# Performance work log

Hardware: AMD Instinct MI355X
Metric: run time of the kernel (lower is better)

The kernel has to match this reference:

```python
import jax, jax.numpy as jnp
import numpy as np

G = 32          # num graphs
NPG = 512       # nodes per graph
EPG = 4096      # edges per graph
DN = 128        # node/edge feat dim
DP = 64         # node identifier dim d_p
DE_ID = 64      # type identifier dim d_e
H = 768         # hidden_dim
IN_DIM = DN + 2 * DP + DE_ID  # 320


def setup_inputs() -> dict:
    key = jax.random.key(0)
    ks = jax.random.split(key, 9)
    N = G * NPG
    E = G * EPG
    x = jax.random.normal(ks[0], (N, DN), jnp.float32)
    edge_attr = jax.random.normal(ks[1], (E, DN), jnp.float32)
    P = jax.random.normal(ks[2], (N, DP), jnp.float32)  # ORF node identifiers
    E_V = jax.random.normal(ks[3], (1, DE_ID), jnp.float32) * 0.1
    E_E = jax.random.normal(ks[4], (1, DE_ID), jnp.float32) * 0.1
    W = jax.random.normal(ks[5], (H, IN_DIM), jnp.float32) / np.sqrt(IN_DIM)
    b = jnp.zeros((H,), jnp.float32)
    graph_token = jax.random.normal(ks[6], (1, H), jnp.float32) * 0.1
    # edges stay within their graph and are sorted by graph id
    base = jnp.repeat(jnp.arange(G, dtype=jnp.int32) * NPG, EPG)  # [E]
    src = base + jax.random.randint(ks[7], (E,), 0, NPG, jnp.int32)
    dst = base + jax.random.randint(ks[8], (E,), 0, NPG, jnp.int32)
    edge_index = jnp.stack([src, dst], axis=0)  # [2, E]
    batch = jnp.repeat(jnp.arange(G, dtype=jnp.int32), NPG)  # [N]
    return {
        "x": x, "edge_attr": edge_attr, "P": P,
        "E_V": E_V, "E_E": E_E, "W": W, "b": b, "graph_token": graph_token,
        "edge_index": edge_index, "batch": batch,
        "num_graphs": G, "max_node_num": NPG, "max_edge_num": EPG,
    }


def reference(x, edge_attr, P, E_V, E_E, W, b, graph_token,
              edge_index, batch, num_graphs, max_node_num, max_edge_num):
    N = x.shape[0]
    E = edge_index.shape[1]
    Hd = W.shape[0]
    d_e = E_V.shape[1]

    # node tokens: [x | P | P | E_V] @ W^T + b
    X_v = jnp.concatenate([x, P, P, jnp.broadcast_to(E_V, (N, d_e))], axis=1)
    X_v_proj = X_v @ W.T + b  # [N, H]

    # edge tokens: [edge_attr | P_u | P_v | E_E] @ W^T + b
    P_u = P[edge_index[0]]
    P_v = P[edge_index[1]]
    X_e = jnp.concatenate([edge_attr, P_u, P_v, jnp.broadcast_to(E_E, (E, d_e))], axis=1)
    X_e_proj = X_e @ W.T + b  # [E, H]

    # ragged -> padded packing (replaces per-graph python loop)
    ones_n = jnp.ones((N,), jnp.int32)
    node_num = jax.ops.segment_sum(ones_n, batch, num_segments=num_graphs)  # [G]
    node_ptr = jnp.cumsum(node_num) - node_num  # exclusive prefix sum
    node_pos = jnp.arange(N, dtype=jnp.int32) - node_ptr[batch]  # position within graph

    edge_batch = batch[edge_index[0]]  # [E]
    ones_e = jnp.ones((E,), jnp.int32)
    edge_num = jax.ops.segment_sum(ones_e, edge_batch, num_segments=num_graphs)
    edge_ptr = jnp.cumsum(edge_num) - edge_num
    edge_pos = jnp.arange(E, dtype=jnp.int32) - edge_ptr[edge_batch]

    seq_len = 1 + max_node_num + max_edge_num  # +1 for [graph] token
    tokens = jnp.zeros((num_graphs, seq_len, Hd), X_v_proj.dtype)
    tokens = tokens.at[:, 0, :].set(graph_token[0])
    tokens = tokens.at[batch, 1 + node_pos].set(X_v_proj)
    tokens = tokens.at[edge_batch, 1 + max_node_num + edge_pos].set(X_e_proj)

    attention_masks = jnp.zeros((num_graphs, seq_len), bool)
    attention_masks = attention_masks.at[:, 0].set(True)
    attention_masks = attention_masks.at[batch, 1 + node_pos].set(True)
    attention_masks = attention_masks.at[edge_batch, 1 + max_node_num + edge_pos].set(True)

    return tokens, attention_masks
```

## Files before the change

### kernel.cpp

```cpp
#include <hip/hip_runtime.h>
#include <stdint.h>

#define NG   32
#define NPG  512
#define EPG  4096
#define DN   128
#define DP   64
#define NN   (NG*NPG)
#define NE   (NG*EPG)
#define KD   320
#define HD   768
#define SEQ  (1+NPG+EPG)
#define TOK_ELEMS ((size_t)NG*SEQ*HD)
#define MASK_ELEMS ((size_t)NG*SEQ)

#define APAD 328
#define BPAD 40

typedef unsigned short u16;
typedef __attribute__((ext_vector_type(8))) __bf16 bf16x8;
typedef __attribute__((ext_vector_type(8))) short  s16x8;
typedef __attribute__((ext_vector_type(4))) float  f32x4;

__device__ __forceinline__ u16 f2bf(float f) {
    uint32_t u = __builtin_bit_cast(uint32_t, f);
    u += 0x7fffu + ((u >> 16) & 1u);
    return (u16)(u >> 16);
}

__global__ void ptr_k(const int* __restrict__ batch, const int* __restrict__ eidx,
                      int* __restrict__ nptr, int* __restrict__ eptr) {
    int t = threadIdx.x;
    if (t < NG) {
        int g = t, lo = 0, hi = NN;
        while (lo < hi) { int mid = (lo + hi) >> 1; if (batch[mid] < g) lo = mid + 1; else hi = mid; }
        nptr[g] = lo;
    } else if (t < 2 * NG) {
        int g = t - NG, lo = 0, hi = NE;
        while (lo < hi) { int mid = (lo + hi) >> 1; if (batch[eidx[mid]] < g) lo = mid + 1; else hi = mid; }
        eptr[g] = lo;
    }
}

__global__ void wconv_k(const float* __restrict__ W, u16* __restrict__ Wb) {
    int i = blockIdx.x * 256 + threadIdx.x;
    if (i < KD * HD) Wb[i] = f2bf(W[i]);
}

__global__ void aux_k(const float* __restrict__ gt, float* __restrict__ out) {
    size_t i = (size_t)blockIdx.x * 256 + threadIdx.x;
    if (i < (size_t)NG * HD) {
        int g = (int)(i / HD), c = (int)(i % HD);
        out[(size_t)g * SEQ * HD + c] = gt[c];
    } else {
        size_t m = i - (size_t)NG * HD;
        if (m < MASK_ELEMS) out[TOK_ELEMS + m] = 1.0f;
    }
}

__global__ __launch_bounds__(256)
void gemm_scatter(const float* __restrict__ x,  const float* __restrict__ ea,
                  const float* __restrict__ P,  const float* __restrict__ EV,
                  const float* __restrict__ EEv,const float* __restrict__ bias,
                  const int* __restrict__ eidx, const int* __restrict__ batch,
                  const u16* __restrict__ Wb,   const int* __restrict__ nptr,
                  const int* __restrict__ eptr, float* __restrict__ out)
{
    __shared__ __align__(16) u16 a_full[64 * APAD];
    __shared__ __align__(16) u16 b_tile[128 * BPAD];
    __shared__ int info_src[64], info_pu[64], info_pv[64], info_orow[64];

    const int tid = threadIdx.x;
    const int r0  = blockIdx.x * 64;
    const bool isNode = (r0 < NN);
    const float* feat = isNode ? x  : ea;
    const float* idv  = isNode ? EV : EEv;

    if (tid < 64) {
        int r = r0 + tid;
        if (isNode) {
            int g = batch[r];
            info_src[tid] = r; info_pu[tid] = r; info_pv[tid] = r;
            info_orow[tid] = g * SEQ + 1 + (r - nptr[g]);
        } else {
            int e = r - NN;
            int s = eidx[e], d = eidx[NE + e];
            int g = batch[s];
            info_src[tid] = e; info_pu[tid] = s; info_pv[tid] = d;
            info_orow[tid] = g * SEQ + 1 + NPG + (e - eptr[g]);
        }
    }
    __syncthreads();

    {
        const int arow = tid >> 2;
        const int ac   = (tid & 3) * 8;
        const int fsrc = info_src[arow];
        const int pu   = info_pu[arow];
        const int pv   = info_pv[arow];
        #pragma unroll
        for (int s = 0; s < KD / 32; ++s) {
            const int kg = s * 32 + ac;
            const float* sp;
            if      (s < 4) sp = feat + (size_t)fsrc * DN + kg;
            else if (s < 6) sp = P + (size_t)pu * DP + (kg - DN);
            else if (s < 8) sp = P + (size_t)pv * DP + (kg - DN - DP);
            else            sp = idv + (kg - DN - 2 * DP);
            f32x4 f0 = *reinterpret_cast<const f32x4*>(sp);
            f32x4 f1 = *reinterpret_cast<const f32x4*>(sp + 4);
            s16x8 v;
            v[0]=(short)f2bf(f0[0]); v[1]=(short)f2bf(f0[1]);
            v[2]=(short)f2bf(f0[2]); v[3]=(short)f2bf(f0[3]);
            v[4]=(short)f2bf(f1[0]); v[5]=(short)f2bf(f1[1]);
            v[6]=(short)f2bf(f1[2]); v[7]=(short)f2bf(f1[3]);
            *reinterpret_cast<s16x8*>(&a_full[arow * APAD + kg]) = v;
        }
    }

    const int lane = tid & 63;
    const int wid  = tid >> 6;
    const int lrow = lane & 15;
    const int lq   = lane >> 4;

    size_t my_row_base[4];
    #pragma unroll
    for (int j = 0; j < 4; ++j)
        my_row_base[j] = (size_t)info_orow[wid * 16 + lq * 4 + j] * HD;

    for (int nt = 0; nt < HD / 128; ++nt) {
        const int n0 = nt * 128;
        f32x4 acc[8];
        #pragma unroll
        for (int i = 0; i < 8; ++i) acc[i] = (f32x4)0.f;

        for (int kt = 0; kt < KD / 32; ++kt) {
            #pragma unroll
            for (int t = 0; t < 2; ++t) {
                int u  = tid + t * 256;
                int nl = u >> 2;
                int c  = (u & 3) * 8;
                *reinterpret_cast<s16x8*>(&b_tile[nl * BPAD + c]) =
                    *reinterpret_cast<const s16x8*>(&Wb[(size_t)(n0 + nl) * KD + kt * 32 + c]);
            }
            __syncthreads();
            bf16x8 af = *reinterpret_cast<const bf16x8*>(
                &a_full[(wid * 16 + lrow) * APAD + kt * 32 + lq * 8]);
            #pragma unroll
            for (int ni = 0; ni < 8; ++ni) {
                bf16x8 bf = *reinterpret_cast<const bf16x8*>(
                    &b_tile[(ni * 16 + lrow) * BPAD + lq * 8]);
                acc[ni] = __builtin_amdgcn_mfma_f32_16x16x32_bf16(af, bf, acc[ni], 0, 0, 0);
            }
            __syncthreads();
        }

        #pragma unroll
        for (int ni = 0; ni < 8; ++ni) {
            float bv = bias[n0 + ni * 16 + lrow];
            #pragma unroll
            for (int j = 0; j < 4; ++j)
                out[my_row_base[j] + n0 + ni * 16 + lrow] = acc[ni][j] + bv;
        }
    }
}

extern "C" void kernel_launch(void* const* d_in, const int* in_sizes, int n_in,
                              void* d_out, int out_size, void* d_ws, size_t ws_size,
                              hipStream_t stream) {
    const float* x    = (const float*)d_in[0];
    const float* ea   = (const float*)d_in[1];
    const float* P    = (const float*)d_in[2];
    const float* EV   = (const float*)d_in[3];
    const float* EEv  = (const float*)d_in[4];
    const float* W    = (const float*)d_in[5];
    const float* bias = (const float*)d_in[6];
    const float* gt   = (const float*)d_in[7];
    const int* eidx   = (const int*)d_in[8];
    const int* batch  = (const int*)d_in[9];

    float* out = (float*)d_out;
    u16* Wb  = (u16*)d_ws;
    int* ints = (int*)((char*)d_ws + (size_t)KD * HD * 2);
    int *nptr = ints, *eptr = ints + 32;

    ptr_k<<<1, 64, 0, stream>>>(batch, eidx, nptr, eptr);
    wconv_k<<<(KD * HD + 255) / 256, 256, 0, stream>>>(W, Wb);
    aux_k<<<(int)(((size_t)NG * HD + MASK_ELEMS + 255) / 256), 256, 0, stream>>>(gt, out);
    gemm_scatter<<<dim3((NN + NE) / 64), 256, 0, stream>>>(
        x, ea, P, EV, EEv, bias, eidx, batch, Wb, nptr, eptr, out);
}
```

Before: 201.0 us.

## Keep A fragments in registers, double-buffer swizzled B tiles with prefetch

Each lane now loads its A row fragments directly from global memory into registers (10 bf16x8), which drops the padded A staging array from LDS. The B tile moves into a double-buffered, XOR-swizzled LDS layout, and the next tile is prefetched into registers a step ahead, so one barrier per k-step replaces two. The goal is less LDS traffic and fewer syncs, with global W loads overlapping MFMA work. The costs are higher register pressure and reliance on a manual waitcnt and barrier. Output offsets also shrink to int, which still fits the output size.

After: 178.2 us. 1.13x faster.

```diff
diff --git a/kernel.cpp b/kernel.cpp
--- a/kernel.cpp
+++ b/kernel.cpp
@@ -14,9 +14,6 @@
 #define TOK_ELEMS ((size_t)NG*SEQ*HD)
 #define MASK_ELEMS ((size_t)NG*SEQ)
 
-#define APAD 328
-#define BPAD 40
-
 typedef unsigned short u16;
 typedef __attribute__((ext_vector_type(8))) __bf16 bf16x8;
 typedef __attribute__((ext_vector_type(8))) short  s16x8;
@@ -26,6 +23,10 @@
     uint32_t u = __builtin_bit_cast(uint32_t, f);
     u += 0x7fffu + ((u >> 16) & 1u);
     return (u16)(u >> 16);
+}
+
+__device__ __forceinline__ int b_off(int row, int kb) {
+    return ((row >> 1) << 7) + ((row & 1) << 6) + (kb ^ (((row >> 1) & 3) << 4));
 }
 
 __global__ void ptr_k(const int* __restrict__ batch, const int* __restrict__ eidx,
@@ -66,8 +67,7 @@
                   const u16* __restrict__ Wb,   const int* __restrict__ nptr,
                   const int* __restrict__ eptr, float* __restrict__ out)
 {
-    __shared__ __align__(16) u16 a_full[64 * APAD];
-    __shared__ __align__(16) u16 b_tile[128 * BPAD];
+    __shared__ __align__(16) char b_lds[2][8192];
     __shared__ int info_src[64], info_pu[64], info_pv[64], info_orow[64];
 
     const int tid = threadIdx.x;
@@ -92,66 +92,77 @@
     }
     __syncthreads();
 
-    {
-        const int arow = tid >> 2;
-        const int ac   = (tid & 3) * 8;
-        const int fsrc = info_src[arow];
-        const int pu   = info_pu[arow];
-        const int pv   = info_pv[arow];
-        #pragma unroll
-        for (int s = 0; s < KD / 32; ++s) {
-            const int kg = s * 32 + ac;
-            const float* sp;
-            if      (s < 4) sp = feat + (size_t)fsrc * DN + kg;
-            else if (s < 6) sp = P + (size_t)pu * DP + (kg - DN);
-            else if (s < 8) sp = P + (size_t)pv * DP + (kg - DN - DP);
-            else            sp = idv + (kg - DN - 2 * DP);
-            f32x4 f0 = *reinterpret_cast<const f32x4*>(sp);
-            f32x4 f1 = *reinterpret_cast<const f32x4*>(sp + 4);
-            s16x8 v;
-            v[0]=(short)f2bf(f0[0]); v[1]=(short)f2bf(f0[1]);
-            v[2]=(short)f2bf(f0[2]); v[3]=(short)f2bf(f0[3]);
-            v[4]=(short)f2bf(f1[0]); v[5]=(short)f2bf(f1[1]);
-            v[6]=(short)f2bf(f1[2]); v[7]=(short)f2bf(f1[3]);
-            *reinterpret_cast<s16x8*>(&a_full[arow * APAD + kg]) = v;
-        }
-    }
-
     const int lane = tid & 63;
     const int wid  = tid >> 6;
     const int lrow = lane & 15;
     const int lq   = lane >> 4;
-
-    size_t my_row_base[4];
+    const int arow = wid * 16 + lrow;
+
+    const int fsrc = info_src[arow];
+    const int pu   = info_pu[arow];
+    const int pv   = info_pv[arow];
+    bf16x8 afr[10];
+    #pragma unroll
+    for (int s = 0; s < 10; ++s) {
+        const int kg = s * 32 + lq * 8;
+        const float* sp;
+        if      (s < 4) sp = feat + (size_t)fsrc * DN + kg;
+        else if (s < 6) sp = P + (size_t)pu * DP + (kg - DN);
+        else if (s < 8) sp = P + (size_t)pv * DP + (kg - DN - DP);
+        else            sp = idv + (kg - DN - 2 * DP);
+        f32x4 f0 = *reinterpret_cast<const f32x4*>(sp);
+        f32x4 f1 = *reinterpret_cast<const f32x4*>(sp + 4);
+        s16x8 v;
+        v[0]=(short)f2bf(f0[0]); v[1]=(short)f2bf(f0[1]);
+        v[2]=(short)f2bf(f0[2]); v[3]=(short)f2bf(f0[3]);
+        v[4]=(short)f2bf(f1[0]); v[5]=(short)f2bf(f1[1]);
+        v[6]=(short)f2bf(f1[2]); v[7]=(short)f2bf(f1[3]);
+        afr[s] = __builtin_bit_cast(bf16x8, v);
+    }
+
+    int obase[4];
     #pragma unroll
     for (int j = 0; j < 4; ++j)
-        my_row_base[j] = (size_t)info_orow[wid * 16 + lq * 4 + j] * HD;
-
-    for (int nt = 0; nt < HD / 128; ++nt) {
+        obase[j] = info_orow[wid * 16 + lq * 4 + j] * HD;
+
+    const int nl0 = tid >> 2;
+    const int nl1 = nl0 + 64;
+    const int kb  = (tid & 3) * 16;
+
+    s16x8 pre0, pre1;
+    {
+        pre0 = *reinterpret_cast<const s16x8*>(Wb + (size_t)nl0 * KD + kb / 2);
+        pre1 = *reinterpret_cast<const s16x8*>(Wb + (size_t)nl1 * KD + kb / 2);
+    }
+
+    for (int nt = 0; nt < 6; ++nt) {
         const int n0 = nt * 128;
         f32x4 acc[8];
         #pragma unroll
         for (int i = 0; i < 8; ++i) acc[i] = (f32x4)0.f;
 
-        for (int kt = 0; kt < KD / 32; ++kt) {
-            #pragma unroll
-            for (int t = 0; t < 2; ++t) {
-                int u  = tid + t * 256;
-                int nl = u >> 2;
-                int c  = (u & 3) * 8;
-                *reinterpret_cast<s16x8*>(&b_tile[nl * BPAD + c]) =
-                    *reinterpret_cast<const s16x8*>(&Wb[(size_t)(n0 + nl) * KD + kt * 32 + c]);
+        #pragma unroll
+        for (int kt = 0; kt < 10; ++kt) {
+            char* bb = b_lds[kt & 1];
+            *reinterpret_cast<s16x8*>(bb + b_off(nl0, kb)) = pre0;
+            *reinterpret_cast<s16x8*>(bb + b_off(nl1, kb)) = pre1;
+            {
+                int t  = nt * 10 + kt;
+                int tn = (t < 59) ? t + 1 : 59;
+                int ntn = tn / 10, ktn = tn - ntn * 10;
+                const u16* q = Wb + (size_t)(ntn * 128) * KD + ktn * 32 + kb / 2;
+                pre0 = *reinterpret_cast<const s16x8*>(q + (size_t)nl0 * KD);
+                pre1 = *reinterpret_cast<const s16x8*>(q + (size_t)nl1 * KD);
             }
-            __syncthreads();
-            bf16x8 af = *reinterpret_cast<const bf16x8*>(
-                &a_full[(wid * 16 + lrow) * APAD + kt * 32 + lq * 8]);
+            asm volatile("s_waitcnt lgkmcnt(0)" ::: "memory");
+            __builtin_amdgcn_sched_barrier(0);
+            __builtin_amdgcn_s_barrier();
             #pragma unroll
             for (int ni = 0; ni < 8; ++ni) {
                 bf16x8 bf = *reinterpret_cast<const bf16x8*>(
-                    &b_tile[(ni * 16 + lrow) * BPAD + lq * 8]);
-                acc[ni] = __builtin_amdgcn_mfma_f32_16x16x32_bf16(af, bf, acc[ni], 0, 0, 0);
+                    bb + b_off(ni * 16 + lrow, lq * 16));
+                acc[ni] = __builtin_amdgcn_mfma_f32_16x16x32_bf16(afr[kt], bf, acc[ni], 0, 0, 0);
             }
-            __syncthreads();
         }
 
         #pragma unroll
@@ -159,7 +170,7 @@
             float bv = bias[n0 + ni * 16 + lrow];
             #pragma unroll
             for (int j = 0; j < 4; ++j)
-                out[my_row_base[j] + n0 + ni * 16 + lrow] = acc[ni][j] + bv;
+                out[obase[j] + n0 + ni * 16 + lrow] = acc[ni][j] + bv;
         }
     }
 }
```
